# Performance work log

Measured on AMD Instinct MI355X. Metric: run time of the kernel, lower is better.

The kernel has to match this reference:

```python
import jax, jax.numpy as jnp
import numpy as np

N = 100000
E = 1600000
F_IN = 128
F_OUT = 128


def setup_inputs() -> dict:
    key = jax.random.key(0)
    k1, k2, k3, k4 = jax.random.split(key, 4)
    x = jax.random.normal(k1, (N, F_IN), dtype=jnp.float32)
    edge_index = jax.random.randint(k2, (2, E), 0, N, dtype=jnp.int64)
    # GCNConv params (glorot weight, zero bias as in PyG defaults)
    limit = float(np.sqrt(6.0 / (F_IN + F_OUT)))
    W = jax.random.uniform(k3, (F_IN, F_OUT), minval=-limit, maxval=limit, dtype=jnp.float32)
    b = jnp.zeros((F_OUT,), dtype=jnp.float32)
    return {"x": x, "edge_index": edge_index, "W": W, "b": b}


def reference(x, edge_index, W, b):
    n = x.shape[0]
    # add self-loops
    loops = jnp.arange(n, dtype=edge_index.dtype)
    src = jnp.concatenate([edge_index[0], loops])  # source nodes j
    dst = jnp.concatenate([edge_index[1], loops])  # target nodes i
    # symmetric normalization: deg over incoming edges (targets), weight 1
    deg = jax.ops.segment_sum(jnp.ones_like(dst, dtype=x.dtype), dst, num_segments=n)
    dinv = jnp.where(deg > 0, jax.lax.rsqrt(deg), 0.0)
    norm = dinv[src] * dinv[dst]  # [E+N]
    # linear transform then message passing
    h = x @ W  # [N, F_OUT]
    msgs = h[src] * norm[:, None]  # gather + scale, [E+N, F_OUT]
    out = jax.ops.segment_sum(msgs, dst, num_segments=n)  # scatter-add
    return out + b
```

## Files before the change

### kernel.cpp

```cpp
#include <hip/hip_runtime.h>

#define FDIM 128
#define NBMAX 512
#define EPB 4096

typedef __attribute__((ext_vector_type(8))) short bf16x8;
typedef __attribute__((ext_vector_type(4))) float f32x4;

__device__ __forceinline__ unsigned short f2bf(float f) {
    unsigned int u = __float_as_uint(f);
    unsigned int r = u + 0x7fffu + ((u >> 16) & 1u);
    return (unsigned short)(r >> 16);
}

__global__ __launch_bounds__(256) void k_prep(const int* __restrict__ dst,
                                              int* __restrict__ bcnt,
                                              const float* __restrict__ W,
                                              unsigned short* __restrict__ whi,
                                              int e, int ebl) {
    __shared__ int h[NBMAX];
    if ((int)blockIdx.x < ebl) {
        for (int i = threadIdx.x; i < NBMAX; i += 256) h[i] = 0;
        __syncthreads();
        int base = blockIdx.x * EPB;
        int end = min(base + EPB, e);
        for (int i = base + threadIdx.x; i < end; i += 256) atomicAdd(&h[dst[i] >> 8], 1);
        __syncthreads();
        for (int i = threadIdx.x; i < NBMAX; i += 256) {
            int c = h[i];
            if (c) atomicAdd(&bcnt[i], c);
        }
    } else {
        int id = ((int)blockIdx.x - ebl) * 256 + threadIdx.x;
        int k = id >> 7, nn = id & 127;
        whi[nn * FDIM + k] = f2bf(W[id]);
    }
}

__global__ __launch_bounds__(256) void k_main(
    const int* __restrict__ src, const int* __restrict__ dst,
    const int* __restrict__ bcnt,
    int* __restrict__ gcur, unsigned int* __restrict__ coarse,
    const float* __restrict__ x, const unsigned short* __restrict__ whi,
    unsigned short* __restrict__ hs, int e, int n, int ebl) {
    __shared__ unsigned short Bs[FDIM * FDIM];
    __shared__ int cur[NBMAX];
    __shared__ int bb[NBMAX];

    if ((int)blockIdx.x < ebl) {
        int t = threadIdx.x;
        int v0 = bcnt[t], v1 = bcnt[t + 256];
        cur[t] = v0;
        cur[t + 256] = v1;
        __syncthreads();
        for (int off = 1; off < NBMAX; off <<= 1) {
            int a0 = (t >= off) ? cur[t - off] : 0;
            int a1 = (t + 256 >= off) ? cur[t + 256 - off] : 0;
            __syncthreads();
            cur[t] += a0;
            cur[t + 256] += a1;
            __syncthreads();
        }
        bb[t] = cur[t] - v0;
        bb[t + 256] = cur[t + 256] - v1;
        __syncthreads();
        cur[t] = 0;
        cur[t + 256] = 0;
        __syncthreads();
        int base = blockIdx.x * EPB;
        int end = min(base + EPB, e);
        for (int i = base + threadIdx.x; i < end; i += 256) atomicAdd(&cur[dst[i] >> 8], 1);
        __syncthreads();
        for (int i = threadIdx.x; i < NBMAX; i += 256) {
            int c = cur[i];
            cur[i] = c ? (bb[i] + atomicAdd(&gcur[i], c)) : 0;
        }
        __syncthreads();
        for (int i = base + threadIdx.x; i < end; i += 256) {
            int d = dst[i];
            int p = atomicAdd(&cur[d >> 8], 1);
            coarse[p] = ((unsigned)src[i] << 8) | (unsigned)(d & 255);
        }
    } else {
        {
            const float4* g4 = (const float4*)whi;
            float4* l4 = (float4*)Bs;
            for (int i = threadIdx.x; i < 2048; i += 256) {
                int nn = i >> 4;
                int g = i & 15;
                l4[nn * 16 + (g ^ (nn & 15))] = g4[i];
            }
        }
        __syncthreads();

        const int lane = threadIdx.x & 63;
        const int wid = threadIdx.x >> 6;
        const int m = lane & 15;
        const int quad = lane >> 4;
        const int row0 = ((int)blockIdx.x - ebl) * 64 + wid * 16;

        int rowA = row0 + m;
        if (rowA >= n) rowA = n - 1;
        const float* xr = x + (size_t)rowA * FDIM;

        f32x4 acc[8];
        #pragma unroll
        for (int ct = 0; ct < 8; ++ct) acc[ct] = (f32x4){0.f, 0.f, 0.f, 0.f};

        #pragma unroll
        for (int kc = 0; kc < 4; ++kc) {
            const int kb = kc * 32 + quad * 8;
            float4 xa = *(const float4*)(xr + kb);
            float4 xb = *(const float4*)(xr + kb + 4);
            float v[8] = {xa.x, xa.y, xa.z, xa.w, xb.x, xb.y, xb.z, xb.w};
            bf16x8 ahi, alo;
            #pragma unroll
            for (int j = 0; j < 8; ++j) {
                unsigned short hh = f2bf(v[j]);
                ahi[j] = (short)hh;
                alo[j] = (short)f2bf(v[j] - __uint_as_float(((unsigned)hh) << 16));
            }
            const int g = kc * 4 + quad;
            #pragma unroll
            for (int ct = 0; ct < 8; ++ct) {
                int nidx = ct * 16 + m;
                const bf16x8 bhi = *(const bf16x8*)(Bs + (size_t)nidx * FDIM + (g ^ m) * 8);
                acc[ct] = __builtin_amdgcn_mfma_f32_16x16x32_bf16(ahi, bhi, acc[ct], 0, 0, 0);
                acc[ct] = __builtin_amdgcn_mfma_f32_16x16x32_bf16(alo, bhi, acc[ct], 0, 0, 0);
            }
        }

        #pragma unroll
        for (int r = 0; r < 4; ++r) {
            int row = row0 + quad * 4 + r;
            if (row >= n) continue;
            unsigned short* hrow = hs + (size_t)row * FDIM;
            #pragma unroll
            for (int ct = 0; ct < 8; ++ct) hrow[ct * 16 + m] = f2bf(acc[ct][r]);
        }
    }
}

__global__ __launch_bounds__(256) void k_bfin(const unsigned int* __restrict__ coarse,
                                              const int* __restrict__ bcnt,
                                              float* __restrict__ dinv,
                                              int* __restrict__ row_start,
                                              int* __restrict__ ebuf, int n, int e) {
    __shared__ int bsc[NBMAX];
    __shared__ int ld[256];
    __shared__ int sc[256];
    __shared__ int cur[256];
    int b = blockIdx.x;
    int tt = threadIdx.x;
    bsc[tt] = bcnt[tt];
    bsc[tt + 256] = bcnt[tt + 256];
    __syncthreads();
    for (int off = 1; off < NBMAX; off <<= 1) {
        int a0 = (tt >= off) ? bsc[tt - off] : 0;
        int a1 = (tt + 256 >= off) ? bsc[tt + 256 - off] : 0;
        __syncthreads();
        bsc[tt] += a0;
        bsc[tt + 256] += a1;
        __syncthreads();
    }
    int s = (b > 0) ? bsc[b - 1] : 0;
    int t = bsc[b];
    if (b == 0 && tt == 0) row_start[n] = e;

    ld[tt] = 0;
    __syncthreads();
    for (int i = s + tt; i < t; i += 256) atomicAdd(&ld[coarse[i] & 255u], 1);
    __syncthreads();
    int v = ld[tt];
    sc[tt] = v;
    __syncthreads();
    for (int off = 1; off < 256; off <<= 1) {
        int tv = (tt >= off) ? sc[tt - off] : 0;
        __syncthreads();
        sc[tt] += tv;
        __syncthreads();
    }
    int rs = s + sc[tt] - v;
    cur[tt] = rs;
    int node = b * 256 + tt;
    if (node < n) {
        dinv[node] = rsqrtf((float)(v + 1));
        row_start[node] = rs;
    }
    __syncthreads();
    for (int i = s + tt; i < t; i += 256) {
        unsigned int p = coarse[i];
        int pos = atomicAdd(&cur[p & 255u], 1);
        ebuf[pos] = (int)(p >> 8);
    }
}

__global__ __launch_bounds__(256, 8) void k_gather(
    const unsigned short* __restrict__ hs, const int* __restrict__ ebuf,
    const int* __restrict__ row_start, const float* __restrict__ dinv,
    const float* __restrict__ bias, float* __restrict__ out, int n) {
    const int lane = threadIdx.x & 63;
    const int gw = (int)blockIdx.x * 4 + (threadIdx.x >> 6);
    const int nw = (int)gridDim.x * 4;

    const unsigned int* __restrict__ hl = (const unsigned int*)hs + lane;
    const float2 bb = ((const float2*)bias)[lane];

    for (int i = gw; i < n; i += nw) {
        int beg = row_start[i];
        int end = row_start[i + 1];
        float di = dinv[i];

        unsigned int u = hl[(unsigned)i << 6];
        float ax = di * __uint_as_float(u << 16);
        float ay = di * __uint_as_float(u & 0xffff0000u);
        float bx = 0.f, by = 0.f;

        int j = beg;
        int stop8 = j + ((end - j) & ~7);
        if (j < stop8) {
            int s0 = ebuf[j + 0], s1 = ebuf[j + 1], s2 = ebuf[j + 2], s3 = ebuf[j + 3];
            int s4 = ebuf[j + 4], s5 = ebuf[j + 5], s6 = ebuf[j + 6], s7 = ebuf[j + 7];
            j += 8;
            while (j < stop8) {
                unsigned int u0 = hl[(unsigned)s0 << 6], u1 = hl[(unsigned)s1 << 6];
                unsigned int u2 = hl[(unsigned)s2 << 6], u3 = hl[(unsigned)s3 << 6];
                unsigned int u4 = hl[(unsigned)s4 << 6], u5 = hl[(unsigned)s5 << 6];
                unsigned int u6 = hl[(unsigned)s6 << 6], u7 = hl[(unsigned)s7 << 6];
                float d0 = dinv[s0], d1 = dinv[s1], d2 = dinv[s2], d3 = dinv[s3];
                float d4 = dinv[s4], d5 = dinv[s5], d6 = dinv[s6], d7 = dinv[s7];
                int t0 = ebuf[j + 0], t1 = ebuf[j + 1], t2 = ebuf[j + 2], t3 = ebuf[j + 3];
                int t4 = ebuf[j + 4], t5 = ebuf[j + 5], t6 = ebuf[j + 6], t7 = ebuf[j + 7];
                ax = fmaf(d0, __uint_as_float(u0 << 16), ax);
                ay = fmaf(d0, __uint_as_float(u0 & 0xffff0000u), ay);
                bx = fmaf(d1, __uint_as_float(u1 << 16), bx);
                by = fmaf(d1, __uint_as_float(u1 & 0xffff0000u), by);
                ax = fmaf(d2, __uint_as_float(u2 << 16), ax);
                ay = fmaf(d2, __uint_as_float(u2 & 0xffff0000u), ay);
                bx = fmaf(d3, __uint_as_float(u3 << 16), bx);
                by = fmaf(d3, __uint_as_float(u3 & 0xffff0000u), by);
                ax = fmaf(d4, __uint_as_float(u4 << 16), ax);
                ay = fmaf(d4, __uint_as_float(u4 & 0xffff0000u), ay);
                bx = fmaf(d5, __uint_as_float(u5 << 16), bx);
                by = fmaf(d5, __uint_as_float(u5 & 0xffff0000u), by);
                ax = fmaf(d6, __uint_as_float(u6 << 16), ax);
                ay = fmaf(d6, __uint_as_float(u6 & 0xffff0000u), ay);
                bx = fmaf(d7, __uint_as_float(u7 << 16), bx);
                by = fmaf(d7, __uint_as_float(u7 & 0xffff0000u), by);
                s0 = t0; s1 = t1; s2 = t2; s3 = t3;
                s4 = t4; s5 = t5; s6 = t6; s7 = t7;
                j += 8;
            }
            {
                unsigned int u0 = hl[(unsigned)s0 << 6], u1 = hl[(unsigned)s1 << 6];
                unsigned int u2 = hl[(unsigned)s2 << 6], u3 = hl[(unsigned)s3 << 6];
                unsigned int u4 = hl[(unsigned)s4 << 6], u5 = hl[(unsigned)s5 << 6];
                unsigned int u6 = hl[(unsigned)s6 << 6], u7 = hl[(unsigned)s7 << 6];
                float d0 = dinv[s0], d1 = dinv[s1], d2 = dinv[s2], d3 = dinv[s3];
                float d4 = dinv[s4], d5 = dinv[s5], d6 = dinv[s6], d7 = dinv[s7];
                ax = fmaf(d0, __uint_as_float(u0 << 16), ax);
                ay = fmaf(d0, __uint_as_float(u0 & 0xffff0000u), ay);
                bx = fmaf(d1, __uint_as_float(u1 << 16), bx);
                by = fmaf(d1, __uint_as_float(u1 & 0xffff0000u), by);
                ax = fmaf(d2, __uint_as_float(u2 << 16), ax);
                ay = fmaf(d2, __uint_as_float(u2 & 0xffff0000u), ay);
                bx = fmaf(d3, __uint_as_float(u3 << 16), bx);
                by = fmaf(d3, __uint_as_float(u3 & 0xffff0000u), by);
                ax = fmaf(d4, __uint_as_float(u4 << 16), ax);
                ay = fmaf(d4, __uint_as_float(u4 & 0xffff0000u), ay);
                bx = fmaf(d5, __uint_as_float(u5 << 16), bx);
                by = fmaf(d5, __uint_as_float(u5 & 0xffff0000u), by);
                ax = fmaf(d6, __uint_as_float(u6 << 16), ax);
                ay = fmaf(d6, __uint_as_float(u6 & 0xffff0000u), ay);
                bx = fmaf(d7, __uint_as_float(u7 << 16), bx);
                by = fmaf(d7, __uint_as_float(u7 & 0xffff0000u), by);
            }
        }
        for (; j + 3 < end; j += 4) {
            int s0 = ebuf[j], s1 = ebuf[j + 1], s2 = ebuf[j + 2], s3 = ebuf[j + 3];
            float d0 = dinv[s0], d1 = dinv[s1], d2 = dinv[s2], d3 = dinv[s3];
            unsigned int u0 = hl[(unsigned)s0 << 6];
            unsigned int u1 = hl[(unsigned)s1 << 6];
            unsigned int u2 = hl[(unsigned)s2 << 6];
            unsigned int u3 = hl[(unsigned)s3 << 6];
            ax = fmaf(d0, __uint_as_float(u0 << 16), ax);
            ay = fmaf(d0, __uint_as_float(u0 & 0xffff0000u), ay);
            bx = fmaf(d1, __uint_as_float(u1 << 16), bx);
            by = fmaf(d1, __uint_as_float(u1 & 0xffff0000u), by);
            ax = fmaf(d2, __uint_as_float(u2 << 16), ax);
            ay = fmaf(d2, __uint_as_float(u2 & 0xffff0000u), ay);
            bx = fmaf(d3, __uint_as_float(u3 << 16), bx);
            by = fmaf(d3, __uint_as_float(u3 & 0xffff0000u), by);
        }
        for (; j < end; ++j) {
            int s0 = ebuf[j];
            float d0 = dinv[s0];
            unsigned int u0 = hl[(unsigned)s0 << 6];
            ax = fmaf(d0, __uint_as_float(u0 << 16), ax);
            ay = fmaf(d0, __uint_as_float(u0 & 0xffff0000u), ay);
        }
        ax += bx;
        ay += by;

        float2 r = make_float2(fmaf(ax, di, bb.x), fmaf(ay, di, bb.y));
        ((float2*)(out + (size_t)i * FDIM))[lane] = r;
    }
}

extern "C" void kernel_launch(void* const* d_in, const int* in_sizes, int n_in,
                              void* d_out, int out_size, void* d_ws, size_t ws_size,
                              hipStream_t stream) {
    const float* x  = (const float*)d_in[0];
    const int*   ei = (const int*)d_in[1];
    const float* W  = (const float*)d_in[2];
    const float* b  = (const float*)d_in[3];

    const int n = in_sizes[0] / FDIM;
    const int e = in_sizes[1] / 2;
    const int* src = ei;
    const int* dst = ei + e;
    float* out = (float*)d_out;

    const int nb = (n + 255) >> 8;
    const int ebl = (e + EPB - 1) / EPB;
    const int gemmbl = (n + 63) / 64;

    char* ws = (char*)d_ws;
    size_t off = 0;
    auto alloc = [&](size_t bytes) {
        char* p = ws + off;
        off += (bytes + 511) & ~(size_t)511;
        return p;
    };
    float*          dinv      = (float*)alloc((size_t)n * 4);
    int*            row_start = (int*)alloc((size_t)(n + 1) * 4);
    int*            bcnt      = (int*)alloc((size_t)NBMAX * 4);
    int*            gcur      = (int*)alloc((size_t)NBMAX * 4);
    unsigned short* whi       = (unsigned short*)alloc((size_t)FDIM * FDIM * 2);
    unsigned int*   coarse    = (unsigned int*)alloc((size_t)e * 4);
    int*            ebuf      = (int*)alloc((size_t)e * 4);
    unsigned short* hs        = (unsigned short*)alloc((size_t)n * FDIM * 2);

    hipMemsetAsync(bcnt, 0, (size_t)NBMAX * 4 * 2, stream);

    k_prep<<<ebl + 64, 256, 0, stream>>>(dst, bcnt, W, whi, e, ebl);
    k_main<<<ebl + gemmbl, 256, 0, stream>>>(src, dst, bcnt, gcur, coarse, x, whi, hs, e, n, ebl);
    k_bfin<<<nb, 256, 0, stream>>>(coarse, bcnt, dinv, row_start, ebuf, n, e);
    {
        int blocks = (n + 3) / 4;
        if (blocks > 2048) blocks = 2048;
        k_gather<<<blocks, 256, 0, stream>>>(hs, ebuf, row_start, dinv, b, out, n);
    }
}
```

Before: 235.8 us.

## Stage coarse bucket scatter in LDS and pad global bucket counters

The coarse partition pass now sorts each block's edges by bucket in shared memory, using a local prefix scan, and then writes them to global memory in bucket-contiguous runs. The goal is coalesced writes in place of scattered 4-byte stores. The global bucket counters (bcnt, gcur) are also padded to 16 ints apart so atomics on different buckets fall on separate cache lines. This adds an extra block-wide scan, more LDS traffic and barriers, and reuses the GEMM's shared buffer through a union.

```diff
diff --git a/kernel.cpp b/kernel.cpp
--- a/kernel.cpp
+++ b/kernel.cpp
@@ -3,6 +3,7 @@
 #define FDIM 128
 #define NBMAX 512
 #define EPB 4096
+#define CPAD 16
 
 typedef __attribute__((ext_vector_type(8))) short bf16x8;
 typedef __attribute__((ext_vector_type(4))) float f32x4;
@@ -28,7 +29,7 @@
         __syncthreads();
         for (int i = threadIdx.x; i < NBMAX; i += 256) {
             int c = h[i];
-            if (c) atomicAdd(&bcnt[i], c);
+            if (c) atomicAdd(&bcnt[i * CPAD], c);
         }
     } else {
         int id = ((int)blockIdx.x - ebl) * 256 + threadIdx.x;
@@ -40,51 +41,89 @@
 __global__ __launch_bounds__(256) void k_main(
     const int* __restrict__ src, const int* __restrict__ dst,
     const int* __restrict__ bcnt,
-    int* __restrict__ gcur, unsigned int* __restrict__ coarse,
+    int* __restrict__ gcur,
+    unsigned int* __restrict__ coarse,
     const float* __restrict__ x, const unsigned short* __restrict__ whi,
     unsigned short* __restrict__ hs, int e, int n, int ebl) {
-    __shared__ unsigned short Bs[FDIM * FDIM];
+    union ShU {
+        unsigned short Bs[FDIM * FDIM];
+        struct {
+            int sval[EPB];
+            unsigned short sbkt[EPB];
+            int loff[NBMAX];
+            int gbs[NBMAX];
+        } sc;
+    };
+    __shared__ ShU S;
     __shared__ int cur[NBMAX];
     __shared__ int bb[NBMAX];
 
     if ((int)blockIdx.x < ebl) {
-        int t = threadIdx.x;
-        int v0 = bcnt[t], v1 = bcnt[t + 256];
-        cur[t] = v0;
-        cur[t + 256] = v1;
+        const int t = threadIdx.x;
+        int* scr = S.sc.sval;
+
+        int v0 = bcnt[t * CPAD], v1 = bcnt[(t + 256) * CPAD];
+        scr[t] = v0;
+        scr[t + 256] = v1;
         __syncthreads();
         for (int off = 1; off < NBMAX; off <<= 1) {
-            int a0 = (t >= off) ? cur[t - off] : 0;
-            int a1 = (t + 256 >= off) ? cur[t + 256 - off] : 0;
+            int a0 = (t >= off) ? scr[t - off] : 0;
+            int a1 = (t + 256 >= off) ? scr[t + 256 - off] : 0;
             __syncthreads();
-            cur[t] += a0;
-            cur[t + 256] += a1;
+            scr[t] += a0;
+            scr[t + 256] += a1;
             __syncthreads();
         }
-        bb[t] = cur[t] - v0;
-        bb[t + 256] = cur[t + 256] - v1;
-        __syncthreads();
+        bb[t] = scr[t] - v0;
+        bb[t + 256] = scr[t + 256] - v1;
+
         cur[t] = 0;
         cur[t + 256] = 0;
         __syncthreads();
         int base = blockIdx.x * EPB;
         int end = min(base + EPB, e);
-        for (int i = base + threadIdx.x; i < end; i += 256) atomicAdd(&cur[dst[i] >> 8], 1);
-        __syncthreads();
-        for (int i = threadIdx.x; i < NBMAX; i += 256) {
-            int c = cur[i];
-            cur[i] = c ? (bb[i] + atomicAdd(&gcur[i], c)) : 0;
-        }
-        __syncthreads();
-        for (int i = base + threadIdx.x; i < end; i += 256) {
+        int cnt = end - base;
+        for (int i = base + t; i < end; i += 256) atomicAdd(&cur[dst[i] >> 8], 1);
+        __syncthreads();
+
+        int c0 = cur[t], c1 = cur[t + 256];
+        scr[t] = c0;
+        scr[t + 256] = c1;
+        __syncthreads();
+        for (int off = 1; off < NBMAX; off <<= 1) {
+            int a0 = (t >= off) ? scr[t - off] : 0;
+            int a1 = (t + 256 >= off) ? scr[t + 256 - off] : 0;
+            __syncthreads();
+            scr[t] += a0;
+            scr[t + 256] += a1;
+            __syncthreads();
+        }
+        S.sc.loff[t] = scr[t] - c0;
+        S.sc.loff[t + 256] = scr[t + 256] - c1;
+        S.sc.gbs[t] = bb[t] + (c0 ? atomicAdd(&gcur[t * CPAD], c0) : 0);
+        S.sc.gbs[t + 256] = bb[t + 256] + (c1 ? atomicAdd(&gcur[(t + 256) * CPAD], c1) : 0);
+        cur[t] = 0;
+        cur[t + 256] = 0;
+        __syncthreads();
+
+        for (int i = base + t; i < end; i += 256) {
             int d = dst[i];
-            int p = atomicAdd(&cur[d >> 8], 1);
-            coarse[p] = ((unsigned)src[i] << 8) | (unsigned)(d & 255);
+            int b = d >> 8;
+            int lp = atomicAdd(&cur[b], 1);
+            int pos = S.sc.loff[b] + lp;
+            S.sc.sval[pos] = (int)(((unsigned)src[i] << 8) | (unsigned)(d & 255));
+            S.sc.sbkt[pos] = (unsigned short)b;
+        }
+        __syncthreads();
+
+        for (int s = t; s < cnt; s += 256) {
+            int b = S.sc.sbkt[s];
+            coarse[S.sc.gbs[b] + (s - S.sc.loff[b])] = (unsigned)S.sc.sval[s];
         }
     } else {
         {
             const float4* g4 = (const float4*)whi;
-            float4* l4 = (float4*)Bs;
+            float4* l4 = (float4*)S.Bs;
             for (int i = threadIdx.x; i < 2048; i += 256) {
                 int nn = i >> 4;
                 int g = i & 15;
@@ -124,7 +163,7 @@
             #pragma unroll
             for (int ct = 0; ct < 8; ++ct) {
                 int nidx = ct * 16 + m;
-                const bf16x8 bhi = *(const bf16x8*)(Bs + (size_t)nidx * FDIM + (g ^ m) * 8);
+                const bf16x8 bhi = *(const bf16x8*)(S.Bs + (size_t)nidx * FDIM + (g ^ m) * 8);
                 acc[ct] = __builtin_amdgcn_mfma_f32_16x16x32_bf16(ahi, bhi, acc[ct], 0, 0, 0);
                 acc[ct] = __builtin_amdgcn_mfma_f32_16x16x32_bf16(alo, bhi, acc[ct], 0, 0, 0);
             }
@@ -152,8 +191,8 @@
     __shared__ int cur[256];
     int b = blockIdx.x;
     int tt = threadIdx.x;
-    bsc[tt] = bcnt[tt];
-    bsc[tt + 256] = bcnt[tt + 256];
+    bsc[tt] = bcnt[tt * CPAD];
+    bsc[tt + 256] = bcnt[(tt + 256) * CPAD];
     __syncthreads();
     for (int off = 1; off < NBMAX; off <<= 1) {
         int a0 = (tt >= off) ? bsc[tt - off] : 0;
@@ -334,14 +373,14 @@
     };
     float*          dinv      = (float*)alloc((size_t)n * 4);
     int*            row_start = (int*)alloc((size_t)(n + 1) * 4);
-    int*            bcnt      = (int*)alloc((size_t)NBMAX * 4);
-    int*            gcur      = (int*)alloc((size_t)NBMAX * 4);
+    int*            bcnt      = (int*)alloc((size_t)NBMAX * CPAD * 4);
+    int*            gcur      = (int*)alloc((size_t)NBMAX * CPAD * 4);
     unsigned short* whi       = (unsigned short*)alloc((size_t)FDIM * FDIM * 2);
     unsigned int*   coarse    = (unsigned int*)alloc((size_t)e * 4);
     int*            ebuf      = (int*)alloc((size_t)e * 4);
     unsigned short* hs        = (unsigned short*)alloc((size_t)n * FDIM * 2);
 
-    hipMemsetAsync(bcnt, 0, (size_t)NBMAX * 4 * 2, stream);
+    hipMemsetAsync(bcnt, 0, (size_t)NBMAX * CPAD * 4 * 2, stream);
 
     k_prep<<<ebl + 64, 256, 0, stream>>>(dst, bcnt, W, whi, e, ebl);
     k_main<<<ebl + gemmbl, 256, 0, stream>>>(src, dst, bcnt, gcur, coarse, x, whi, hs, e, n, ebl);
```

New measurement: 232.7 us. About the same (-1.3%).

## Replace two-level bucket sort with per-node atomic counting sort and separate GEMM

Applied to the files above, without the earlier changes.

Drops the coarse bucket partition pass and the per-bucket fine sort. Per-node in-degrees are now counted with global atomics in the prep pass, scanned into row offsets, and edges are scattered directly with per-node atomic cursors. The GEMM moves into its own kernel that processes four tiles per block so the weight staging is amortised. This removes the coarse intermediate buffer and one full pass over the edges, but adds heavy global atomic traffic on 100k counters and no longer overlaps the GEMM with the sort.

```diff
diff --git a/kernel.cpp b/kernel.cpp
--- a/kernel.cpp
+++ b/kernel.cpp
@@ -3,6 +3,7 @@
 #define FDIM 128
 #define NBMAX 512
 #define EPB 4096
+#define CPAD 16
 
 typedef __attribute__((ext_vector_type(8))) short bf16x8;
 typedef __attribute__((ext_vector_type(4))) float f32x4;
@@ -13,8 +14,70 @@
     return (unsigned short)(r >> 16);
 }
 
+__device__ __forceinline__ void gemm_tile(int tt, const float* __restrict__ x,
+                                          const unsigned short* Bs,
+                                          unsigned short* __restrict__ hs, int n, int tid) {
+    const int lane = tid & 63;
+    const int wid = tid >> 6;
+    const int m = lane & 15;
+    const int quad = lane >> 4;
+    const int row0 = tt * 64 + wid * 16;
+
+    int rowA = row0 + m;
+    if (rowA >= n) rowA = n - 1;
+    const float* xr = x + (size_t)rowA * FDIM;
+
+    f32x4 acc[8];
+    #pragma unroll
+    for (int ct = 0; ct < 8; ++ct) acc[ct] = (f32x4){0.f, 0.f, 0.f, 0.f};
+
+    #pragma unroll
+    for (int kc = 0; kc < 4; ++kc) {
+        const int kb = kc * 32 + quad * 8;
+        float4 xa = *(const float4*)(xr + kb);
+        float4 xb = *(const float4*)(xr + kb + 4);
+        float v[8] = {xa.x, xa.y, xa.z, xa.w, xb.x, xb.y, xb.z, xb.w};
+        bf16x8 ahi, alo;
+        #pragma unroll
+        for (int j = 0; j < 8; ++j) {
+            unsigned short hh = f2bf(v[j]);
+            ahi[j] = (short)hh;
+            alo[j] = (short)f2bf(v[j] - __uint_as_float(((unsigned)hh) << 16));
+        }
+        const int g = kc * 4 + quad;
+        #pragma unroll
+        for (int ct = 0; ct < 8; ++ct) {
+            int nidx = ct * 16 + m;
+            const bf16x8 bhi = *(const bf16x8*)(Bs + (size_t)nidx * FDIM + (g ^ m) * 8);
+            acc[ct] = __builtin_amdgcn_mfma_f32_16x16x32_bf16(ahi, bhi, acc[ct], 0, 0, 0);
+            acc[ct] = __builtin_amdgcn_mfma_f32_16x16x32_bf16(alo, bhi, acc[ct], 0, 0, 0);
+        }
+    }
+
+    #pragma unroll
+    for (int r = 0; r < 4; ++r) {
+        int row = row0 + quad * 4 + r;
+        if (row >= n) continue;
+        unsigned short* hrow = hs + (size_t)row * FDIM;
+        #pragma unroll
+        for (int ct = 0; ct < 8; ++ct) hrow[ct * 16 + m] = f2bf(acc[ct][r]);
+    }
+}
+
+__device__ __forceinline__ void stage_Bs(const unsigned short* __restrict__ whi,
+                                         unsigned short* Bs, int tid) {
+    const float4* g4 = (const float4*)whi;
+    float4* l4 = (float4*)Bs;
+    for (int i = tid; i < 2048; i += 256) {
+        int nn = i >> 4;
+        int g = i & 15;
+        l4[nn * 16 + (g ^ (nn & 15))] = g4[i];
+    }
+}
+
 __global__ __launch_bounds__(256) void k_prep(const int* __restrict__ dst,
                                               int* __restrict__ bcnt,
+                                              int* __restrict__ cnt,
                                               const float* __restrict__ W,
                                               unsigned short* __restrict__ whi,
                                               int e, int ebl) {
@@ -24,11 +87,15 @@
         __syncthreads();
         int base = blockIdx.x * EPB;
         int end = min(base + EPB, e);
-        for (int i = base + threadIdx.x; i < end; i += 256) atomicAdd(&h[dst[i] >> 8], 1);
+        for (int i = base + threadIdx.x; i < end; i += 256) {
+            int d = dst[i];
+            atomicAdd(&h[d >> 8], 1);
+            atomicAdd(&cnt[d], 1);
+        }
         __syncthreads();
         for (int i = threadIdx.x; i < NBMAX; i += 256) {
             int c = h[i];
-            if (c) atomicAdd(&bcnt[i], c);
+            if (c) atomicAdd(&bcnt[i * CPAD], c);
         }
     } else {
         int id = ((int)blockIdx.x - ebl) * 256 + threadIdx.x;
@@ -37,123 +104,17 @@
     }
 }
 
-__global__ __launch_bounds__(256) void k_main(
-    const int* __restrict__ src, const int* __restrict__ dst,
-    const int* __restrict__ bcnt,
-    int* __restrict__ gcur, unsigned int* __restrict__ coarse,
-    const float* __restrict__ x, const unsigned short* __restrict__ whi,
-    unsigned short* __restrict__ hs, int e, int n, int ebl) {
-    __shared__ unsigned short Bs[FDIM * FDIM];
-    __shared__ int cur[NBMAX];
-    __shared__ int bb[NBMAX];
-
-    if ((int)blockIdx.x < ebl) {
-        int t = threadIdx.x;
-        int v0 = bcnt[t], v1 = bcnt[t + 256];
-        cur[t] = v0;
-        cur[t + 256] = v1;
-        __syncthreads();
-        for (int off = 1; off < NBMAX; off <<= 1) {
-            int a0 = (t >= off) ? cur[t - off] : 0;
-            int a1 = (t + 256 >= off) ? cur[t + 256 - off] : 0;
-            __syncthreads();
-            cur[t] += a0;
-            cur[t + 256] += a1;
-            __syncthreads();
-        }
-        bb[t] = cur[t] - v0;
-        bb[t + 256] = cur[t + 256] - v1;
-        __syncthreads();
-        cur[t] = 0;
-        cur[t + 256] = 0;
-        __syncthreads();
-        int base = blockIdx.x * EPB;
-        int end = min(base + EPB, e);
-        for (int i = base + threadIdx.x; i < end; i += 256) atomicAdd(&cur[dst[i] >> 8], 1);
-        __syncthreads();
-        for (int i = threadIdx.x; i < NBMAX; i += 256) {
-            int c = cur[i];
-            cur[i] = c ? (bb[i] + atomicAdd(&gcur[i], c)) : 0;
-        }
-        __syncthreads();
-        for (int i = base + threadIdx.x; i < end; i += 256) {
-            int d = dst[i];
-            int p = atomicAdd(&cur[d >> 8], 1);
-            coarse[p] = ((unsigned)src[i] << 8) | (unsigned)(d & 255);
-        }
-    } else {
-        {
-            const float4* g4 = (const float4*)whi;
-            float4* l4 = (float4*)Bs;
-            for (int i = threadIdx.x; i < 2048; i += 256) {
-                int nn = i >> 4;
-                int g = i & 15;
-                l4[nn * 16 + (g ^ (nn & 15))] = g4[i];
-            }
-        }
-        __syncthreads();
-
-        const int lane = threadIdx.x & 63;
-        const int wid = threadIdx.x >> 6;
-        const int m = lane & 15;
-        const int quad = lane >> 4;
-        const int row0 = ((int)blockIdx.x - ebl) * 64 + wid * 16;
-
-        int rowA = row0 + m;
-        if (rowA >= n) rowA = n - 1;
-        const float* xr = x + (size_t)rowA * FDIM;
-
-        f32x4 acc[8];
-        #pragma unroll
-        for (int ct = 0; ct < 8; ++ct) acc[ct] = (f32x4){0.f, 0.f, 0.f, 0.f};
-
-        #pragma unroll
-        for (int kc = 0; kc < 4; ++kc) {
-            const int kb = kc * 32 + quad * 8;
-            float4 xa = *(const float4*)(xr + kb);
-            float4 xb = *(const float4*)(xr + kb + 4);
-            float v[8] = {xa.x, xa.y, xa.z, xa.w, xb.x, xb.y, xb.z, xb.w};
-            bf16x8 ahi, alo;
-            #pragma unroll
-            for (int j = 0; j < 8; ++j) {
-                unsigned short hh = f2bf(v[j]);
-                ahi[j] = (short)hh;
-                alo[j] = (short)f2bf(v[j] - __uint_as_float(((unsigned)hh) << 16));
-            }
-            const int g = kc * 4 + quad;
-            #pragma unroll
-            for (int ct = 0; ct < 8; ++ct) {
-                int nidx = ct * 16 + m;
-                const bf16x8 bhi = *(const bf16x8*)(Bs + (size_t)nidx * FDIM + (g ^ m) * 8);
-                acc[ct] = __builtin_amdgcn_mfma_f32_16x16x32_bf16(ahi, bhi, acc[ct], 0, 0, 0);
-                acc[ct] = __builtin_amdgcn_mfma_f32_16x16x32_bf16(alo, bhi, acc[ct], 0, 0, 0);
-            }
-        }
-
-        #pragma unroll
-        for (int r = 0; r < 4; ++r) {
-            int row = row0 + quad * 4 + r;
-            if (row >= n) continue;
-            unsigned short* hrow = hs + (size_t)row * FDIM;
-            #pragma unroll
-            for (int ct = 0; ct < 8; ++ct) hrow[ct * 16 + m] = f2bf(acc[ct][r]);
-        }
-    }
-}
-
-__global__ __launch_bounds__(256) void k_bfin(const unsigned int* __restrict__ coarse,
-                                              const int* __restrict__ bcnt,
+__global__ __launch_bounds__(256) void k_scan(const int* __restrict__ bcnt,
+                                              int* __restrict__ cnt,
                                               float* __restrict__ dinv,
                                               int* __restrict__ row_start,
-                                              int* __restrict__ ebuf, int n, int e) {
+                                              int n, int e) {
     __shared__ int bsc[NBMAX];
-    __shared__ int ld[256];
     __shared__ int sc[256];
-    __shared__ int cur[256];
     int b = blockIdx.x;
     int tt = threadIdx.x;
-    bsc[tt] = bcnt[tt];
-    bsc[tt + 256] = bcnt[tt + 256];
+    bsc[tt] = bcnt[tt * CPAD];
+    bsc[tt + 256] = bcnt[(tt + 256) * CPAD];
     __syncthreads();
     for (int off = 1; off < NBMAX; off <<= 1) {
         int a0 = (tt >= off) ? bsc[tt - off] : 0;
@@ -164,14 +125,9 @@
         __syncthreads();
     }
     int s = (b > 0) ? bsc[b - 1] : 0;
-    int t = bsc[b];
-    if (b == 0 && tt == 0) row_start[n] = e;
-
-    ld[tt] = 0;
-    __syncthreads();
-    for (int i = s + tt; i < t; i += 256) atomicAdd(&ld[coarse[i] & 255u], 1);
-    __syncthreads();
-    int v = ld[tt];
+
+    int node = b * 256 + tt;
+    int v = cnt[node];
     sc[tt] = v;
     __syncthreads();
     for (int off = 1; off < 256; off <<= 1) {
@@ -181,17 +137,38 @@
         __syncthreads();
     }
     int rs = s + sc[tt] - v;
-    cur[tt] = rs;
-    int node = b * 256 + tt;
     if (node < n) {
+        row_start[node] = rs;
+        cnt[node] = rs;
         dinv[node] = rsqrtf((float)(v + 1));
-        row_start[node] = rs;
-    }
+    }
+    if (b == 0 && tt == 0) row_start[n] = e;
+}
+
+__global__ __launch_bounds__(256) void k_scat(const int* __restrict__ src,
+                                              const int* __restrict__ dst,
+                                              int* __restrict__ cnt,
+                                              int* __restrict__ ebuf, int e) {
+    int stride = (int)gridDim.x * 256;
+    for (int i = (int)blockIdx.x * 256 + threadIdx.x; i < e; i += stride) {
+        int d = dst[i];
+        int pos = atomicAdd(&cnt[d], 1);
+        ebuf[pos] = src[i];
+    }
+}
+
+__global__ __launch_bounds__(256) void k_gemm(const float* __restrict__ x,
+                                              const unsigned short* __restrict__ whi,
+                                              unsigned short* __restrict__ hs,
+                                              int n, int ntiles) {
+    __shared__ unsigned short Bs[FDIM * FDIM];
+    stage_Bs(whi, Bs, threadIdx.x);
     __syncthreads();
-    for (int i = s + tt; i < t; i += 256) {
-        unsigned int p = coarse[i];
-        int pos = atomicAdd(&cur[p & 255u], 1);
-        ebuf[pos] = (int)(p >> 8);
+    int t0 = (int)blockIdx.x * 4;
+    #pragma unroll 1
+    for (int k = 0; k < 4; ++k) {
+        int t = t0 + k;
+        if (t < ntiles) gemm_tile(t, x, Bs, hs, n, threadIdx.x);
     }
 }
 
@@ -323,7 +300,8 @@
 
     const int nb = (n + 255) >> 8;
     const int ebl = (e + EPB - 1) / EPB;
-    const int gemmbl = (n + 63) / 64;
+    const int ntiles = (n + 63) / 64;
+    const int gemmbl = (ntiles + 3) / 4;
 
     char* ws = (char*)d_ws;
     size_t off = 0;
@@ -334,18 +312,18 @@
     };
     float*          dinv      = (float*)alloc((size_t)n * 4);
     int*            row_start = (int*)alloc((size_t)(n + 1) * 4);
-    int*            bcnt      = (int*)alloc((size_t)NBMAX * 4);
-    int*            gcur      = (int*)alloc((size_t)NBMAX * 4);
+    int*            bcnt      = (int*)alloc((size_t)NBMAX * CPAD * 4);
+    int*            cnt       = (int*)alloc((size_t)nb * 256 * 4);
     unsigned short* whi       = (unsigned short*)alloc((size_t)FDIM * FDIM * 2);
-    unsigned int*   coarse    = (unsigned int*)alloc((size_t)e * 4);
     int*            ebuf      = (int*)alloc((size_t)e * 4);
     unsigned short* hs        = (unsigned short*)alloc((size_t)n * FDIM * 2);
 
-    hipMemsetAsync(bcnt, 0, (size_t)NBMAX * 4 * 2, stream);
-
-    k_prep<<<ebl + 64, 256, 0, stream>>>(dst, bcnt, W, whi, e, ebl);
-    k_main<<<ebl + gemmbl, 256, 0, stream>>>(src, dst, bcnt, gcur, coarse, x, whi, hs, e, n, ebl);
-    k_bfin<<<nb, 256, 0, stream>>>(coarse, bcnt, dinv, row_start, ebuf, n, e);
+    hipMemsetAsync(bcnt, 0, (size_t)NBMAX * CPAD * 4 + (size_t)nb * 256 * 4, stream);
+
+    k_prep<<<ebl + 64, 256, 0, stream>>>(dst, bcnt, cnt, W, whi, e, ebl);
+    k_scan<<<nb, 256, 0, stream>>>(bcnt, cnt, dinv, row_start, n, e);
+    k_scat<<<1024, 256, 0, stream>>>(src, dst, cnt, ebuf, e);
+    k_gemm<<<gemmbl, 256, 0, stream>>>(x, whi, hs, n, ntiles);
     {
         int blocks = (n + 3) / 4;
         if (blocks > 2048) blocks = 2048;
```

Result: slower. 386.7 us (+64.0%).
